# Optimization experiments

Measured on AMD Instinct MI355X. Metric: run time of the kernel, lower is better.

The kernel has to match this reference:

```python
import jax, jax.numpy as jnp
import numpy as np

N_HEAD = 16
D_K = 64
D_V = 64
D_MODEL = 1024
EPS = 1e-6
NEG = -1e9


def layer_norm(x, gamma, beta):
    mu = jnp.mean(x, axis=-1, keepdims=True)
    var = jnp.var(x, axis=-1, keepdims=True)
    return (x - mu) * jax.lax.rsqrt(var + EPS) * gamma + beta


def setup_inputs() -> dict:
    key = jax.random.key(0)
    ks = jax.random.split(key, 8)
    B, L = 2, 2048
    q = jax.random.normal(ks[0], (B, L, D_MODEL), dtype=jnp.float32)
    k = jax.random.normal(ks[1], (B, L, D_MODEL), dtype=jnp.float32)
    v = jax.random.normal(ks[2], (B, L, D_MODEL), dtype=jnp.float32)
    mask = jnp.ones((L, L), dtype=jnp.int32)
    s = 1.0 / np.sqrt(D_MODEL)
    w_q = jax.random.normal(ks[3], (N_HEAD * D_K, D_MODEL), dtype=jnp.float32) * s
    w_k = jax.random.normal(ks[4], (N_HEAD * D_K, D_MODEL), dtype=jnp.float32) * s
    w_v = jax.random.normal(ks[5], (N_HEAD * D_V, D_MODEL), dtype=jnp.float32) * s
    w_o = jax.random.normal(ks[6], (D_MODEL, N_HEAD * D_V), dtype=jnp.float32) * s
    ln_g = jnp.ones((D_MODEL,), dtype=jnp.float32)
    ln_b = jnp.zeros((D_MODEL,), dtype=jnp.float32)
    return {"q": q, "k": k, "v": v, "mask": mask,
            "w_q": w_q, "w_k": w_k, "w_v": w_v, "w_o": w_o,
            "ln_g": ln_g, "ln_b": ln_b}


def reference(q, k, v, mask, w_q, w_k, w_v, w_o, ln_g, ln_b):
    B, Lq, _ = q.shape
    Lk = k.shape[1]
    residual = q
    qn = layer_norm(q, ln_g, ln_b)
    # projections (nn.Linear: x @ W^T), reshape to [B, H, L, d]
    Q = (qn @ w_q.T).reshape(B, Lq, N_HEAD, D_K).transpose(0, 2, 1, 3)
    K = (k @ w_k.T).reshape(B, Lk, N_HEAD, D_K).transpose(0, 2, 1, 3)
    V = (v @ w_v.T).reshape(B, Lk, N_HEAD, D_V).transpose(0, 2, 1, 3)
    temp = jnp.asarray(D_K ** 0.5, dtype=Q.dtype)
    attn = jnp.einsum('bhqd,bhkd->bhqk', Q / temp, K)
    attn = jnp.where(mask[None, None] == 0, jnp.asarray(NEG, attn.dtype), attn)
    attn = jax.nn.softmax(attn, axis=-1)  # dropout is identity in eval
    out = jnp.einsum('bhqk,bhkd->bhqd', attn, V)
    out = out.transpose(0, 2, 1, 3).reshape(B, Lq, N_HEAD * D_V)
    out = out @ w_o.T
    return out + residual
```

## Files before the change

### kernel.cpp

```cpp
#include <hip/hip_runtime.h>
#include <stdint.h>

typedef __attribute__((ext_vector_type(8))) short bf16x8;
typedef __attribute__((ext_vector_type(4))) short s16x4;
typedef __attribute__((ext_vector_type(4))) float f32x4;

__device__ __forceinline__ ushort f2bf(float f) {
  union { float f; uint32_t u; } c; c.f = f;
  uint32_t r = (c.u + 0x7fffu + ((c.u >> 16) & 1u)) >> 16;
  return (ushort)r;
}

__device__ __forceinline__ void gload16(const void* g, void* l) {
  __builtin_amdgcn_global_load_lds(
      (const __attribute__((address_space(1))) void*)g,
      (__attribute__((address_space(3))) void*)l, 16, 0, 0);
}

__device__ __forceinline__ unsigned lds_addr(const void* p) {
  return (unsigned)(uintptr_t)(__attribute__((address_space(3))) const char*)p;
}

__device__ __forceinline__ uint32_t cvtpk(float lo, float hi) {
  uint32_t d;
  asm("v_cvt_pk_bf16_f32 %0, %1, %2" : "=v"(d) : "v"(lo), "v"(hi));
  return d;
}

__global__ __launch_bounds__(256) void prep_kernel(
    const float* __restrict__ q, const float* __restrict__ k,
    const float* __restrict__ v, const float* __restrict__ w_q,
    const float* __restrict__ w_k, const float* __restrict__ w_v,
    const float* __restrict__ w_o, const float* __restrict__ ln_g,
    const float* __restrict__ ln_b,
    ushort* __restrict__ qn, ushort* __restrict__ kb, ushort* __restrict__ vb,
    ushort* __restrict__ wqb, ushort* __restrict__ wkb,
    ushort* __restrict__ wvb, ushort* __restrict__ wob) {
  const int bid = blockIdx.x;
  const int t = threadIdx.x;
  if (bid < 4096) {
    const int row = bid;
    const float4 val = ((const float4*)(q + (size_t)row * 1024))[t];
    float s  = val.x + val.y + val.z + val.w;
    float s2 = val.x*val.x + val.y*val.y + val.z*val.z + val.w*val.w;
    #pragma unroll
    for (int off = 1; off < 64; off <<= 1) {
      s  += __shfl_xor(s,  off);
      s2 += __shfl_xor(s2, off);
    }
    __shared__ float red[8];
    const int wave = t >> 6, lane = t & 63;
    if (lane == 0) { red[wave*2] = s; red[wave*2+1] = s2; }
    __syncthreads();
    s  = red[0] + red[2] + red[4] + red[6];
    s2 = red[1] + red[3] + red[5] + red[7];
    const float mu = s * (1.0f/1024.0f);
    const float var = s2 * (1.0f/1024.0f) - mu*mu;
    const float rs = rsqrtf(var + 1e-6f);
    const float4 gg = ((const float4*)ln_g)[t];
    const float4 bb = ((const float4*)ln_b)[t];
    ushort4 o;
    o.x = f2bf((val.x - mu) * rs * gg.x + bb.x);
    o.y = f2bf((val.y - mu) * rs * gg.y + bb.y);
    o.z = f2bf((val.z - mu) * rs * gg.z + bb.z);
    o.w = f2bf((val.w - mu) * rs * gg.w + bb.w);
    ((ushort4*)(qn + (size_t)row * 1024))[t] = o;
    return;
  }
  const float* in; ushort* out; int i;
  if (bid < 12288) {
    const int idx = bid - 4096;
    const bool isv = idx >= 4096;
    in  = isv ? v : k;
    out = isv ? vb : kb;
    i = (idx & 4095) * 256 + t;
  } else {
    const int idx = bid - 12288;
    const int w = idx >> 10;
    in  = w == 0 ? w_q : (w == 1 ? w_k : (w == 2 ? w_v : w_o));
    out = w == 0 ? wqb : (w == 1 ? wkb : (w == 2 ? wvb : wob));
    i = (idx & 1023) * 256 + t;
  }
  const float4 val = ((const float4*)in)[i];
  ushort4 o;
  o.x = f2bf(val.x); o.y = f2bf(val.y); o.z = f2bf(val.z); o.w = f2bf(val.w);
  ((ushort4*)out)[i] = o;
}

__global__ __launch_bounds__(256) void mask_flags(
    const int* __restrict__ mask, int* __restrict__ flags) {
  const int qt = blockIdx.y, kt = blockIdx.x;
  const int t = threadIdx.x;
  const int* p = mask + (size_t)(qt * 64 + (t >> 2)) * 2048 + kt * 64 + (t & 3) * 16;
  int ok = 1;
  #pragma unroll
  for (int i = 0; i < 4; i++) {
    const int4 m = ((const int4*)p)[i];
    ok &= (m.x != 0) & (m.y != 0) & (m.z != 0) & (m.w != 0);
  }
  __shared__ int sok;
  if (t == 0) sok = 1;
  __syncthreads();
  if (!ok) atomicAnd(&sok, 0);
  __syncthreads();
  if (t == 0) flags[qt * 32 + kt] = sok;
}

__global__ __launch_bounds__(256, 3) void gemm3(
    const ushort* __restrict__ A0, const ushort* __restrict__ W0, ushort* __restrict__ C0,
    const ushort* __restrict__ A1, const ushort* __restrict__ W1, ushort* __restrict__ C1,
    const ushort* __restrict__ A2, const ushort* __restrict__ W2, ushort* __restrict__ C2,
    float qscale) {
  __shared__ ushort As[3][4096];
  __shared__ ushort Bs[3][4096];
  const int t = threadIdx.x, lane = t & 63, wave = t >> 6;
  const int wr = wave >> 1, wc = wave & 1;
  const int lr = lane & 15, lg = lane >> 4;
  const int lin = blockIdx.x;
  const int swz = (lin & 7) * 96 + (lin >> 3);
  const int brow = ((swz >> 3) & 31) * 128, bcol = (swz & 7) * 128;
  const int z = swz >> 8;
  const ushort* A = z == 0 ? A0 : (z == 1 ? A1 : A2);
  const ushort* W = z == 0 ? W0 : (z == 1 ? W1 : W2);
  ushort*      C = z == 0 ? C0 : (z == 1 ? C1 : C2);
  const float sc = (z == 0) ? qscale : 1.0f;
  f32x4 acc[4][4] = {};
  const int r_ = t >> 2, cx = (t & 3) ^ ((r_ >> 1) & 3);
  const ushort* gA  = A + (size_t)(brow + r_) * 1024 + cx * 8;
  const ushort* gB  = W + (size_t)(bcol + r_) * 1024 + cx * 8;
  const ushort* gA2 = gA + 64 * 1024;
  const ushort* gB2 = gB + 64 * 1024;
  const int woff = wave * 1024;
  char* const la0 = (char*)As[0] + woff;
  char* const la1 = (char*)As[1] + woff;
  char* const la2 = (char*)As[2] + woff;
  char* const lb0 = (char*)Bs[0] + woff;
  char* const lb1 = (char*)Bs[1] + woff;
  char* const lb2 = (char*)Bs[2] + woff;
  const int xA = ((lr >> 1) & 3) * 8;

#define G_ISSUE_U(LA, LB, OFF) { \
    gload16(gA  + (OFF), (LA));        gload16(gA2 + (OFF), (LA) + 4096); \
    gload16(gB  + (OFF), (LB));        gload16(gB2 + (OFF), (LB) + 4096); }

#define G_COMPUTE_U(BI) { \
    const ushort* as_ = As[BI]; \
    const ushort* bs_ = Bs[BI]; \
    bf16x8 af[4], bfr[4]; \
    _Pragma("unroll") for (int i = 0; i < 4; i++) \
      af[i]  = *(const bf16x8*)&as_[(wr*64 + i*16 + lr) * 32 + ((lg*8) ^ xA)]; \
    _Pragma("unroll") for (int i = 0; i < 4; i++) \
      bfr[i] = *(const bf16x8*)&bs_[(wc*64 + i*16 + lr) * 32 + ((lg*8) ^ xA)]; \
    _Pragma("unroll") for (int mi = 0; mi < 4; mi++) \
      _Pragma("unroll") for (int ni = 0; ni < 4; ni++) \
        acc[mi][ni] = __builtin_amdgcn_mfma_f32_16x16x32_bf16(af[mi], bfr[ni], acc[mi][ni], 0, 0, 0); }

  G_ISSUE_U(la0, lb0, 0);
  G_ISSUE_U(la1, lb1, 32);
  for (int k = 0; k < 10; ++k) {
    asm volatile("s_waitcnt vmcnt(4)" ::: "memory");
    __builtin_amdgcn_s_barrier();
    G_ISSUE_U(la2, lb2, 64);
    G_COMPUTE_U(0);
    asm volatile("s_waitcnt vmcnt(4)" ::: "memory");
    __builtin_amdgcn_s_barrier();
    G_ISSUE_U(la0, lb0, 96);
    G_COMPUTE_U(1);
    asm volatile("s_waitcnt vmcnt(4)" ::: "memory");
    __builtin_amdgcn_s_barrier();
    G_ISSUE_U(la1, lb1, 128);
    G_COMPUTE_U(2);
    gA += 96; gA2 += 96; gB += 96; gB2 += 96;
  }
  asm volatile("s_waitcnt vmcnt(4)" ::: "memory");
  __builtin_amdgcn_s_barrier();
  G_COMPUTE_U(0);
  asm volatile("s_waitcnt vmcnt(0)" ::: "memory");
  __builtin_amdgcn_s_barrier();
  G_COMPUTE_U(1);
#undef G_ISSUE_U
#undef G_COMPUTE_U

  #pragma unroll
  for (int mi = 0; mi < 4; mi++) {
    #pragma unroll
    for (int ni = 0; ni < 4; ni++) {
      #pragma unroll
      for (int r = 0; r < 4; r++) {
        const size_t row = brow + wr*64 + mi*16 + lg*4 + r;
        const size_t col = bcol + wc*64 + ni*16 + lr;
        C[row * 1024 + col] = f2bf(acc[mi][ni][r] * sc);
      }
    }
  }
}

__global__ __launch_bounds__(256) void gemm_bm64(
    const ushort* __restrict__ A, const ushort* __restrict__ W,
    float* __restrict__ Cf, const float* __restrict__ resid) {
  __shared__ ushort As[4][2048];
  __shared__ ushort Bs[4][4096];
  const int t = threadIdx.x, lane = t & 63, wave = t >> 6;
  const int wr = wave >> 1, wc = wave & 1;
  const int lr = lane & 15, lg = lane >> 4;
  const int lin = blockIdx.x;
  const int swz = (lin & 7) * 64 + (lin >> 3);
  const int brow = (swz >> 3) * 64, bcol = (swz & 7) * 128;
  f32x4 acc[2][4] = {};
  const int r_ = t >> 2, cx = (t & 3) ^ ((r_ >> 1) & 3);
  const ushort* gA = A + (size_t)(brow + r_) * 1024 + cx * 8;
  const ushort* gB = W + (size_t)(bcol + r_) * 1024 + cx * 8;
  const int woff = wave * 1024;
  const int xA = ((lr >> 1) & 3) * 8;

#define G_ISSUE(S) { \
    char* la = (char*)As + ((S) & 3) * 4096 + woff; \
    char* lb = (char*)Bs + ((S) & 3) * 8192 + woff; \
    const ushort* ap_ = gA + (S) * 32; \
    const ushort* bp_ = gB + (S) * 32; \
    gload16(ap_, la); \
    gload16(bp_, lb); gload16(bp_ + 64 * 1024, lb + 4096); }

#define G_COMPUTE(S) { \
    const ushort* as_ = As[(S) & 3]; \
    const ushort* bs_ = Bs[(S) & 3]; \
    bf16x8 af[2], bfr[4]; \
    _Pragma("unroll") for (int i = 0; i < 2; i++) \
      af[i]  = *(const bf16x8*)&as_[(wr*32 + i*16 + lr) * 32 + ((lg*8) ^ xA)]; \
    _Pragma("unroll") for (int i = 0; i < 4; i++) \
      bfr[i] = *(const bf16x8*)&bs_[(wc*64 + i*16 + lr) * 32 + ((lg*8) ^ xA)]; \
    _Pragma("unroll") for (int mi = 0; mi < 2; mi++) \
      _Pragma("unroll") for (int ni = 0; ni < 4; ni++) \
        acc[mi][ni] = __builtin_amdgcn_mfma_f32_16x16x32_bf16(af[mi], bfr[ni], acc[mi][ni], 0, 0, 0); }

  G_ISSUE(0); G_ISSUE(1); G_ISSUE(2);
  for (int s = 0; s < 30; ++s) {
    asm volatile("s_waitcnt vmcnt(6)" ::: "memory");
    __builtin_amdgcn_s_barrier();
    if (s < 29) G_ISSUE(s + 3);
    G_COMPUTE(s);
  }
  asm volatile("s_waitcnt vmcnt(3)" ::: "memory");
  __builtin_amdgcn_s_barrier();
  G_COMPUTE(30);
  asm volatile("s_waitcnt vmcnt(0)" ::: "memory");
  __builtin_amdgcn_s_barrier();
  G_COMPUTE(31);
#undef G_ISSUE
#undef G_COMPUTE

  #pragma unroll
  for (int mi = 0; mi < 2; mi++) {
    #pragma unroll
    for (int ni = 0; ni < 4; ni++) {
      #pragma unroll
      for (int r = 0; r < 4; r++) {
        const size_t row = brow + wr*32 + mi*16 + lg*4 + r;
        const size_t col = bcol + wc*64 + ni*16 + lr;
        Cf[row * 1024 + col] = acc[mi][ni][r] + resid[row * 1024 + col];
      }
    }
  }
}

__global__ __launch_bounds__(512, 4) void flash_attn(
    const ushort* __restrict__ Qp, const ushort* __restrict__ Kp,
    const ushort* __restrict__ Vp, const int* __restrict__ mask,
    const int* __restrict__ tflags, ushort* __restrict__ AO) {
  const int L = 2048;
  const int lin = blockIdx.x;
  const int swzb = (lin & 7) * 64 + (lin >> 3);
  const int qb = swzb & 15, h = (swzb >> 4) & 15, b = swzb >> 8;
  const int t = threadIdx.x, lane = t & 63, wave = t >> 6;
  const int l15 = lane & 15, hg = lane >> 4;
  __shared__ ushort Ks[2][8192];
  __shared__ ushort Vs[2][8192];
  const size_t base = (size_t)b * L * 1024 + h * 64;
  const int qw0 = qb * 128 + wave * 16;

  bf16x8 qf[2];
  #pragma unroll
  for (int kc = 0; kc < 2; kc++)
    qf[kc] = *(const bf16x8*)(Qp + base + (size_t)(qw0 + l15) * 1024 + kc*32 + hg*8);

  f32x4 accO[4] = {};
  f32x4 accL = {};
  const bf16x8 onef = {16256, 16256, 16256, 16256, 16256, 16256, 16256, 16256};

  const int r5 = t >> 3;
  const ushort* gK = Kp + base + (size_t)r5 * 1024 + ((t & 7) ^ (r5 & 7)) * 8;
  const int vkv = (t >> 5) * 4 + ((t & 7) >> 1);
  const int vd  = ((t >> 3) & 3) * 16 + (t & 1) * 8;
  const ushort* gV = Vp + base + (size_t)vkv * 1024 + vd;

  const unsigned vbase = lds_addr((const char*)Vs) + hg * 1024 + l15 * 8;

#define STAGE2(P, BUF) { \
    char* kb_ = (char*)Ks[BUF] + wave * 1024; \
    const ushort* gk_ = gK + (size_t)(2*(P)) * 65536; \
    gload16(gk_, kb_);           gload16(gk_ + 65536, kb_ + 8192); \
    char* vb_ = (char*)Vs[BUF] + wave * 1024; \
    const ushort* gv_ = gV + (size_t)(2*(P)) * 65536; \
    gload16(gv_, vb_);           gload16(gv_ + 65536, vb_ + 8192); }

#define TRREAD(VLO, VHI, VA, C) { \
    _Pragma("unroll") for (int dblk = 0; dblk < 4; dblk++) \
      asm volatile("ds_read_b64_tr_b16 %0, %2 offset:%3\n\t" \
                   "ds_read_b64_tr_b16 %1, %2 offset:%4" \
                   : "=v"(VLO[dblk]), "=v"(VHI[dblk]) \
                   : "v"(VA), "i"((C)*4096 + dblk*128), "i"((C)*4096 + dblk*128 + 512) \
                   : "memory"); }

  STAGE2(0, 0);
  const int flagBase = (qb * 2 + (wave >> 2)) * 32;

  for (int p = 0; p < 16; ++p) {
    asm volatile("s_waitcnt vmcnt(0)" ::: "memory");
    __builtin_amdgcn_s_barrier();
    if (p + 1 < 16) { STAGE2(p + 1, (p + 1) & 1); }

    #pragma unroll
    for (int half = 0; half < 2; ++half) {
      const int kvt = 2*p + half;
      const char* KsB = (const char*)Ks[p & 1] + half * 8192;
      const unsigned va = vbase + (p & 1) * 16384 + half * 8192;

      f32x4 s0 = {0.f}, s1 = {0.f}, s2 = {0.f}, s3 = {0.f};
      const int rx16 = (l15 & 7) << 4;
      __builtin_amdgcn_s_setprio(1);
      #pragma unroll
      for (int kc = 0; kc < 2; kc++) {
        const int cb = (kc*64 + hg*16) ^ rx16;
        const bf16x8 k0 = *(const bf16x8*)(KsB + (     l15) * 128 + cb);
        const bf16x8 k1 = *(const bf16x8*)(KsB + (16 + l15) * 128 + cb);
        const bf16x8 k2 = *(const bf16x8*)(KsB + (32 + l15) * 128 + cb);
        const bf16x8 k3 = *(const bf16x8*)(KsB + (48 + l15) * 128 + cb);
        s0 = __builtin_amdgcn_mfma_f32_16x16x32_bf16(k0, qf[kc], s0, 0, 0, 0);
        s1 = __builtin_amdgcn_mfma_f32_16x16x32_bf16(k1, qf[kc], s1, 0, 0, 0);
        s2 = __builtin_amdgcn_mfma_f32_16x16x32_bf16(k2, qf[kc], s2, 0, 0, 0);
        s3 = __builtin_amdgcn_mfma_f32_16x16x32_bf16(k3, qf[kc], s3, 0, 0, 0);
      }
      __builtin_amdgcn_s_setprio(0);

      s16x4 vlo[4], vhi[4];
      TRREAD(vlo, vhi, va, 0);

      if (tflags[flagBase + kvt] == 0) {
        const size_t mrow = (size_t)(qw0 + l15) * L + kvt * 64;
        #pragma unroll
        for (int r = 0; r < 4; ++r) {
          const int kvr = hg*4 + r;
          if (mask[mrow + kvr] == 0)      s0[r] = -1e9f;
          if (mask[mrow + 16 + kvr] == 0) s1[r] = -1e9f;
          if (mask[mrow + 32 + kvr] == 0) s2[r] = -1e9f;
          if (mask[mrow + 48 + kvr] == 0) s3[r] = -1e9f;
        }
      }

      #pragma unroll
      for (int r = 0; r < 4; ++r) {
        s0[r] = __builtin_amdgcn_exp2f(s0[r]);
        s1[r] = __builtin_amdgcn_exp2f(s1[r]);
        s2[r] = __builtin_amdgcn_exp2f(s2[r]);
        s3[r] = __builtin_amdgcn_exp2f(s3[r]);
      }

      union U8 { uint32_t u[4]; bf16x8 v; };
      bf16x8 pa[2];
      #pragma unroll
      for (int c = 0; c < 2; ++c) {
        const f32x4& ta = c ? s2 : s0;
        const f32x4& tb = c ? s3 : s1;
        uint32_t A = cvtpk(ta[0], ta[1]), B = cvtpk(ta[2], ta[3]);
        uint32_t C = cvtpk(tb[0], tb[1]), D = cvtpk(tb[2], tb[3]);
        asm("v_permlane32_swap_b32 %0, %1" : "+v"(A), "+v"(C));
        asm("v_permlane16_swap_b32 %0, %1" : "+v"(A), "+v"(C));
        asm("v_permlane32_swap_b32 %0, %1" : "+v"(B), "+v"(D));
        asm("v_permlane16_swap_b32 %0, %1" : "+v"(B), "+v"(D));
        U8 f; f.u[0] = A; f.u[1] = B; f.u[2] = C; f.u[3] = D;
        pa[c] = f.v;
      }

      asm volatile("s_waitcnt lgkmcnt(0)" ::: "memory");
      __builtin_amdgcn_sched_barrier(0);
      __builtin_amdgcn_s_setprio(1);
      #pragma unroll
      for (int dblk = 0; dblk < 4; dblk++) {
        const bf16x8 bv = __builtin_shufflevector(vlo[dblk], vhi[dblk],
                                                  0, 1, 2, 3, 4, 5, 6, 7);
        accO[dblk] = __builtin_amdgcn_mfma_f32_16x16x32_bf16(pa[0], bv, accO[dblk], 0, 0, 0);
      }
      accL = __builtin_amdgcn_mfma_f32_16x16x32_bf16(pa[0], onef, accL, 0, 0, 0);
      __builtin_amdgcn_s_setprio(0);

      TRREAD(vlo, vhi, va, 1);
      asm volatile("s_waitcnt lgkmcnt(0)" ::: "memory");
      __builtin_amdgcn_sched_barrier(0);
      __builtin_amdgcn_s_setprio(1);
      #pragma unroll
      for (int dblk = 0; dblk < 4; dblk++) {
        const bf16x8 bv = __builtin_shufflevector(vlo[dblk], vhi[dblk],
                                                  0, 1, 2, 3, 4, 5, 6, 7);
        accO[dblk] = __builtin_amdgcn_mfma_f32_16x16x32_bf16(pa[1], bv, accO[dblk], 0, 0, 0);
      }
      accL = __builtin_amdgcn_mfma_f32_16x16x32_bf16(pa[1], onef, accL, 0, 0, 0);
      __builtin_amdgcn_s_setprio(0);
    }
  }

  #pragma unroll
  for (int r = 0; r < 4; ++r) {
    const float inv = 1.0f / accL[r];
    const size_t row = (size_t)b * L + qw0 + hg*4 + r;
    #pragma unroll
    for (int dblk = 0; dblk < 4; dblk++)
      AO[row * 1024 + h*64 + dblk*16 + l15] = f2bf(accO[dblk][r] * inv);
  }
#undef STAGE2
#undef TRREAD
}

extern "C" void kernel_launch(void* const* d_in, const int* in_sizes, int n_in,
                              void* d_out, int out_size, void* d_ws, size_t ws_size,
                              hipStream_t stream) {
  const float* q    = (const float*)d_in[0];
  const float* k    = (const float*)d_in[1];
  const float* v    = (const float*)d_in[2];
  const int*   mask = (const int*)d_in[3];
  const float* w_q  = (const float*)d_in[4];
  const float* w_k  = (const float*)d_in[5];
  const float* w_v  = (const float*)d_in[6];
  const float* w_o  = (const float*)d_in[7];
  const float* ln_g = (const float*)d_in[8];
  const float* ln_b = (const float*)d_in[9];
  float* out = (float*)d_out;

  char* ws = (char*)d_ws;
  const size_t MB = (size_t)1 << 20;
  ushort* qn  = (ushort*)(ws + 0*MB);
  ushort* kb  = (ushort*)(ws + 8*MB);
  ushort* vb  = (ushort*)(ws + 16*MB);
  ushort* wqb = (ushort*)(ws + 24*MB);
  ushort* wkb = (ushort*)(ws + 26*MB);
  ushort* wvb = (ushort*)(ws + 28*MB);
  ushort* wob = (ushort*)(ws + 30*MB);
  ushort* Qp  = (ushort*)(ws + 32*MB);
  ushort* Kp  = (ushort*)(ws + 40*MB);
  ushort* Vp  = (ushort*)(ws + 48*MB);
  ushort* AO  = (ushort*)(ws + 56*MB);
  int* tflags = (int*)(ws + 8*MB);

  const float QSCALE = 0.125f * 1.44269504089f;

  prep_kernel<<<16384, 256, 0, stream>>>(
      q, k, v, w_q, w_k, w_v, w_o, ln_g, ln_b,
      qn, kb, vb, wqb, wkb, wvb, wob);

  gemm3<<<768, 256, 0, stream>>>(
      qn, wqb, Qp, kb, wkb, Kp, vb, wvb, Vp, QSCALE);

  mask_flags<<<dim3(32, 32), 256, 0, stream>>>(mask, tflags);

  flash_attn<<<512, 512, 0, stream>>>(Qp, Kp, Vp, mask, tflags, AO);

  gemm_bm64<<<512, 256, 0, stream>>>(AO, wob, out, q);
}
```

Measured before the change: 124.9 us.

## Double query rows per wave in flash attention to reuse K/V tiles

```diff
diff --git a/kernel.cpp b/kernel.cpp
--- a/kernel.cpp
+++ b/kernel.cpp
@@ -263,28 +263,31 @@
   }
 }
 
-__global__ __launch_bounds__(512, 4) void flash_attn(
+__global__ __launch_bounds__(512) void flash_attn(
     const ushort* __restrict__ Qp, const ushort* __restrict__ Kp,
     const ushort* __restrict__ Vp, const int* __restrict__ mask,
     const int* __restrict__ tflags, ushort* __restrict__ AO) {
   const int L = 2048;
   const int lin = blockIdx.x;
-  const int swzb = (lin & 7) * 64 + (lin >> 3);
-  const int qb = swzb & 15, h = (swzb >> 4) & 15, b = swzb >> 8;
+  const int swzb = (lin & 7) * 32 + (lin >> 3);
+  const int qb = swzb & 7, h = (swzb >> 3) & 15, b = swzb >> 7;
   const int t = threadIdx.x, lane = t & 63, wave = t >> 6;
   const int l15 = lane & 15, hg = lane >> 4;
   __shared__ ushort Ks[2][8192];
   __shared__ ushort Vs[2][8192];
   const size_t base = (size_t)b * L * 1024 + h * 64;
-  const int qw0 = qb * 128 + wave * 16;
-
-  bf16x8 qf[2];
+  const int qw0 = qb * 256 + wave * 32;
+
+  bf16x8 qf[2][2];
   #pragma unroll
-  for (int kc = 0; kc < 2; kc++)
-    qf[kc] = *(const bf16x8*)(Qp + base + (size_t)(qw0 + l15) * 1024 + kc*32 + hg*8);
-
-  f32x4 accO[4] = {};
-  f32x4 accL = {};
+  for (int qt = 0; qt < 2; qt++)
+    #pragma unroll
+    for (int kc = 0; kc < 2; kc++)
+      qf[qt][kc] = *(const bf16x8*)(Qp + base +
+                     (size_t)(qw0 + qt*16 + l15) * 1024 + kc*32 + hg*8);
+
+  f32x4 accO[2][4] = {};
+  f32x4 accL[2] = {};
   const bf16x8 onef = {16256, 16256, 16256, 16256, 16256, 16256, 16256, 16256};
 
   const int r5 = t >> 3;
@@ -312,7 +315,7 @@
                    : "memory"); }
 
   STAGE2(0, 0);
-  const int flagBase = (qb * 2 + (wave >> 2)) * 32;
+  const int flagBase = (qb * 4 + (wave >> 1)) * 32;
 
   for (int p = 0; p < 16; ++p) {
     asm volatile("s_waitcnt vmcnt(0)" ::: "memory");
@@ -325,7 +328,7 @@
       const char* KsB = (const char*)Ks[p & 1] + half * 8192;
       const unsigned va = vbase + (p & 1) * 16384 + half * 8192;
 
-      f32x4 s0 = {0.f}, s1 = {0.f}, s2 = {0.f}, s3 = {0.f};
+      f32x4 s[2][4] = {};
       const int rx16 = (l15 & 7) << 4;
       __builtin_amdgcn_s_setprio(1);
       #pragma unroll
@@ -335,10 +338,13 @@
         const bf16x8 k1 = *(const bf16x8*)(KsB + (16 + l15) * 128 + cb);
         const bf16x8 k2 = *(const bf16x8*)(KsB + (32 + l15) * 128 + cb);
         const bf16x8 k3 = *(const bf16x8*)(KsB + (48 + l15) * 128 + cb);
-        s0 = __builtin_amdgcn_mfma_f32_16x16x32_bf16(k0, qf[kc], s0, 0, 0, 0);
-        s1 = __builtin_amdgcn_mfma_f32_16x16x32_bf16(k1, qf[kc], s1, 0, 0, 0);
-        s2 = __builtin_amdgcn_mfma_f32_16x16x32_bf16(k2, qf[kc], s2, 0, 0, 0);
-        s3 = __builtin_amdgcn_mfma_f32_16x16x32_bf16(k3, qf[kc], s3, 0, 0, 0);
+        #pragma unroll
+        for (int qt = 0; qt < 2; qt++) {
+          s[qt][0] = __builtin_amdgcn_mfma_f32_16x16x32_bf16(k0, qf[qt][kc], s[qt][0], 0, 0, 0);
+          s[qt][1] = __builtin_amdgcn_mfma_f32_16x16x32_bf16(k1, qf[qt][kc], s[qt][1], 0, 0, 0);
+          s[qt][2] = __builtin_amdgcn_mfma_f32_16x16x32_bf16(k2, qf[qt][kc], s[qt][2], 0, 0, 0);
+          s[qt][3] = __builtin_amdgcn_mfma_f32_16x16x32_bf16(k3, qf[qt][kc], s[qt][3], 0, 0, 0);
+        }
       }
       __builtin_amdgcn_s_setprio(0);
 
@@ -346,39 +352,45 @@
       TRREAD(vlo, vhi, va, 0);
 
       if (tflags[flagBase + kvt] == 0) {
-        const size_t mrow = (size_t)(qw0 + l15) * L + kvt * 64;
         #pragma unroll
-        for (int r = 0; r < 4; ++r) {
-          const int kvr = hg*4 + r;
-          if (mask[mrow + kvr] == 0)      s0[r] = -1e9f;
-          if (mask[mrow + 16 + kvr] == 0) s1[r] = -1e9f;
-          if (mask[mrow + 32 + kvr] == 0) s2[r] = -1e9f;
-          if (mask[mrow + 48 + kvr] == 0) s3[r] = -1e9f;
+        for (int qt = 0; qt < 2; qt++) {
+          const size_t mrow = (size_t)(qw0 + qt*16 + l15) * L + kvt * 64;
+          #pragma unroll
+          for (int r = 0; r < 4; ++r) {
+            const int kvr = hg*4 + r;
+            if (mask[mrow + kvr] == 0)      s[qt][0][r] = -1e9f;
+            if (mask[mrow + 16 + kvr] == 0) s[qt][1][r] = -1e9f;
+            if (mask[mrow + 32 + kvr] == 0) s[qt][2][r] = -1e9f;
+            if (mask[mrow + 48 + kvr] == 0) s[qt][3][r] = -1e9f;
+          }
         }
       }
 
       #pragma unroll
-      for (int r = 0; r < 4; ++r) {
-        s0[r] = __builtin_amdgcn_exp2f(s0[r]);
-        s1[r] = __builtin_amdgcn_exp2f(s1[r]);
-        s2[r] = __builtin_amdgcn_exp2f(s2[r]);
-        s3[r] = __builtin_amdgcn_exp2f(s3[r]);
-      }
+      for (int qt = 0; qt < 2; qt++)
+        #pragma unroll
+        for (int ni = 0; ni < 4; ++ni)
+          #pragma unroll
+          for (int r = 0; r < 4; ++r)
+            s[qt][ni][r] = __builtin_amdgcn_exp2f(s[qt][ni][r]);
 
       union U8 { uint32_t u[4]; bf16x8 v; };
-      bf16x8 pa[2];
-      #pragma unroll
-      for (int c = 0; c < 2; ++c) {
-        const f32x4& ta = c ? s2 : s0;
-        const f32x4& tb = c ? s3 : s1;
-        uint32_t A = cvtpk(ta[0], ta[1]), B = cvtpk(ta[2], ta[3]);
-        uint32_t C = cvtpk(tb[0], tb[1]), D = cvtpk(tb[2], tb[3]);
-        asm("v_permlane32_swap_b32 %0, %1" : "+v"(A), "+v"(C));
-        asm("v_permlane16_swap_b32 %0, %1" : "+v"(A), "+v"(C));
-        asm("v_permlane32_swap_b32 %0, %1" : "+v"(B), "+v"(D));
-        asm("v_permlane16_swap_b32 %0, %1" : "+v"(B), "+v"(D));
-        U8 f; f.u[0] = A; f.u[1] = B; f.u[2] = C; f.u[3] = D;
-        pa[c] = f.v;
+      bf16x8 pa[2][2];
+      #pragma unroll
+      for (int qt = 0; qt < 2; qt++) {
+        #pragma unroll
+        for (int c = 0; c < 2; ++c) {
+          const f32x4& ta = s[qt][2*c];
+          const f32x4& tb = s[qt][2*c + 1];
+          uint32_t A = cvtpk(ta[0], ta[1]), B = cvtpk(ta[2], ta[3]);
+          uint32_t C = cvtpk(tb[0], tb[1]), D = cvtpk(tb[2], tb[3]);
+          asm("v_permlane32_swap_b32 %0, %1" : "+v"(A), "+v"(C));
+          asm("v_permlane16_swap_b32 %0, %1" : "+v"(A), "+v"(C));
+          asm("v_permlane32_swap_b32 %0, %1" : "+v"(B), "+v"(D));
+          asm("v_permlane16_swap_b32 %0, %1" : "+v"(B), "+v"(D));
+          U8 f; f.u[0] = A; f.u[1] = B; f.u[2] = C; f.u[3] = D;
+          pa[qt][c] = f.v;
+        }
       }
 
       asm volatile("s_waitcnt lgkmcnt(0)" ::: "memory");
@@ -388,9 +400,11 @@
       for (int dblk = 0; dblk < 4; dblk++) {
         const bf16x8 bv = __builtin_shufflevector(vlo[dblk], vhi[dblk],
                                                   0, 1, 2, 3, 4, 5, 6, 7);
-        accO[dblk] = __builtin_amdgcn_mfma_f32_16x16x32_bf16(pa[0], bv, accO[dblk], 0, 0, 0);
-      }
-      accL = __builtin_amdgcn_mfma_f32_16x16x32_bf16(pa[0], onef, accL, 0, 0, 0);
+        accO[0][dblk] = __builtin_amdgcn_mfma_f32_16x16x32_bf16(pa[0][0], bv, accO[0][dblk], 0, 0, 0);
+        accO[1][dblk] = __builtin_amdgcn_mfma_f32_16x16x32_bf16(pa[1][0], bv, accO[1][dblk], 0, 0, 0);
+      }
+      accL[0] = __builtin_amdgcn_mfma_f32_16x16x32_bf16(pa[0][0], onef, accL[0], 0, 0, 0);
+      accL[1] = __builtin_amdgcn_mfma_f32_16x16x32_bf16(pa[1][0], onef, accL[1], 0, 0, 0);
       __builtin_amdgcn_s_setprio(0);
 
       TRREAD(vlo, vhi, va, 1);
@@ -401,20 +415,25 @@
       for (int dblk = 0; dblk < 4; dblk++) {
         const bf16x8 bv = __builtin_shufflevector(vlo[dblk], vhi[dblk],
                                                   0, 1, 2, 3, 4, 5, 6, 7);
-        accO[dblk] = __builtin_amdgcn_mfma_f32_16x16x32_bf16(pa[1], bv, accO[dblk], 0, 0, 0);
-      }
-      accL = __builtin_amdgcn_mfma_f32_16x16x32_bf16(pa[1], onef, accL, 0, 0, 0);
+        accO[0][dblk] = __builtin_amdgcn_mfma_f32_16x16x32_bf16(pa[0][1], bv, accO[0][dblk], 0, 0, 0);
+        accO[1][dblk] = __builtin_amdgcn_mfma_f32_16x16x32_bf16(pa[1][1], bv, accO[1][dblk], 0, 0, 0);
+      }
+      accL[0] = __builtin_amdgcn_mfma_f32_16x16x32_bf16(pa[0][1], onef, accL[0], 0, 0, 0);
+      accL[1] = __builtin_amdgcn_mfma_f32_16x16x32_bf16(pa[1][1], onef, accL[1], 0, 0, 0);
       __builtin_amdgcn_s_setprio(0);
     }
   }
 
   #pragma unroll
-  for (int r = 0; r < 4; ++r) {
-    const float inv = 1.0f / accL[r];
-    const size_t row = (size_t)b * L + qw0 + hg*4 + r;
-    #pragma unroll
-    for (int dblk = 0; dblk < 4; dblk++)
-      AO[row * 1024 + h*64 + dblk*16 + l15] = f2bf(accO[dblk][r] * inv);
+  for (int qt = 0; qt < 2; qt++) {
+    #pragma unroll
+    for (int r = 0; r < 4; ++r) {
+      const float inv = 1.0f / accL[qt][r];
+      const size_t row = (size_t)b * L + qw0 + qt*16 + hg*4 + r;
+      #pragma unroll
+      for (int dblk = 0; dblk < 4; dblk++)
+        AO[row * 1024 + h*64 + dblk*16 + l15] = f2bf(accO[qt][dblk][r] * inv);
+    }
   }
 #undef STAGE2
 #undef TRREAD
@@ -461,7 +480,7 @@
 
   mask_flags<<<dim3(32, 32), 256, 0, stream>>>(mask, tflags);
 
-  flash_attn<<<512, 512, 0, stream>>>(Qp, Kp, Vp, mask, tflags, AO);
+  flash_attn<<<256, 512, 0, stream>>>(Qp, Kp, Vp, mask, tflags, AO);
 
   gemm_bm64<<<512, 256, 0, stream>>>(AO, wob, out, q);
 }
```

After: 121.8 us, median of 2. 1.03x faster.
